# Kernel tuning notes

Hardware: AMD Instinct MI355X
Metric: run time of the kernel (lower is better)

## Reference

```python
import jax, jax.numpy as jnp
import numpy as np

B, H, W, ENC = 32, 14, 14, 2048
T = 21            # sequence length; 20 decode steps
V, E, A, L = 10000, 512, 512, 512
P = H * W


def setup_inputs() -> dict:
    key = jax.random.key(0)
    ks = jax.random.split(key, 24)
    g = lambda k, shape, s=0.02: (jax.random.normal(k, shape, jnp.float32) * s)
    return {
        "encoder_output": jax.random.normal(ks[0], (B, H, W, ENC), jnp.float32),
        # tokens in [1, V) so sign/abs length count gives full-length sequences
        "sequences": jax.random.randint(ks[1], (B, T), 1, V).astype(jnp.int64),
        "emb": g(ks[2], (V, E)),
        "Wea": g(ks[3], (ENC, A)), "bea": jnp.zeros((A,), jnp.float32),
        "Wga": g(ks[4], (L, A)),   "bga": jnp.zeros((A,), jnp.float32),
        "Wfa": g(ks[5], (A, 1)),   "bfa": jnp.zeros((1,), jnp.float32),
        "Wl": g(ks[6], (E + ENC, 4 * L)), "Ul": g(ks[7], (L, 4 * L)),
        "bl": jnp.zeros((4 * L,), jnp.float32),
        "Wim": g(ks[8], (ENC, L)), "bim": jnp.zeros((L,), jnp.float32),
        "Wic": g(ks[9], (ENC, L)), "bic": jnp.zeros((L,), jnp.float32),
        "Wb": g(ks[10], (L, ENC)), "bb": jnp.zeros((ENC,), jnp.float32),
        "Wo": g(ks[11], (L, V)),   "bo": jnp.zeros((V,), jnp.float32),
    }


def reference(encoder_output, sequences, emb, Wea, bea, Wga, bga, Wfa, bfa,
              Wl, Ul, bl, Wim, bim, Wic, bic, Wb, bb, Wo, bo):
    # --- sort by descending length (packed-sequence style) ---
    lengths = jnp.sum(jnp.sign(jnp.abs(sequences)), axis=1).astype(jnp.int32)
    order = jnp.argsort(-lengths)
    lengths = lengths[order] - 1                       # number of decode steps per row
    enc = encoder_output[order].reshape(B, P, ENC)     # [B, P, ENC]
    seqs = sequences[order]

    # --- init LSTM states from mean-pooled encoder features ---
    mean = enc.mean(axis=1)                            # [B, ENC]
    h0 = mean @ Wim + bim                              # 'memory_state' (plays role of h)
    c0 = mean @ Wic + bic                              # 'carry_state'  (plays role of c)

    # encoder side of additive attention is time-invariant: hoist out of the loop
    a1 = enc @ Wea + bea                               # [B, P, A]

    steps = T - 1
    toks = seqs[:, :steps].T                           # [steps, B] teacher-forced inputs
    masks = lengths[None, :] > jnp.arange(steps)[:, None]  # [steps, B] active rows

    def step(carry, xs):
        h, c = carry
        tok, m = xs
        # additive attention on carry (cell) state, as in the original code
        a2 = c @ Wga + bga                                         # [B, A]
        e = jnp.squeeze(jax.nn.relu(a1 + a2[:, None, :]) @ Wfa + bfa, -1)  # [B, P]
        alpha = jax.nn.softmax(e, axis=1)
        awe = jnp.einsum('bpe,bp->be', enc, alpha)                 # [B, ENC]
        beta = jax.nn.sigmoid(c @ Wb + bb)                         # gating
        x = jnp.concatenate([emb[tok], awe * beta], axis=1)        # [B, E+ENC]
        # Keras LSTMCell: gate order i, f, g, o
        z = x @ Wl + h @ Ul + bl
        zi, zf, zg, zo = jnp.split(z, 4, axis=1)
        c_new = jax.nn.sigmoid(zf) * c + jax.nn.sigmoid(zi) * jnp.tanh(zg)
        h_new = jax.nn.sigmoid(zo) * jnp.tanh(c_new)
        mf = m[:, None].astype(h.dtype)
        h_new = h_new * mf                 # zero-pad finished rows (packed semantics)
        c_new = c_new * mf
        pred = (c_new @ Wo + bo) * mf      # prediction from carry (cell) state, dropout off
        return (h_new, c_new), (pred, alpha * mf)

    (_, _), (preds, alphas) = jax.lax.scan(step, (h0, c0), (toks, masks))
    return preds.transpose(1, 0, 2), alphas.transpose(1, 0, 2), order
```

## Files before the change

kernel.cpp:

```cpp
#include <hip/hip_runtime.h>
#include <math.h>

#define B_    32
#define T_    21
#define STEPS 20
#define V_    10000
#define E_    512
#define A_    512
#define L_    512
#define P_    196
#define ENC_  2048
#define XW_   3072

#define WS_ORD    0
#define WS_SLEN   32
#define WS_CBUF   64
#define WS_CB0    32832
#define WS_CBALL  36928
#define WS_XB     200768
#define WS_A2S    299072
#define WS_BETA   315456
#define WS_ESH    380992
#define WS_A1B    389184
#define WS_WZP    1994816
#define WS_WCP    5140544
#define WS_WEAT   8384576
#define WS_MEAN   (WS_WZP)
#define WS_PH     (WS_WZP + 65536)

#define OUT_PRED  0
#define OUT_ALPHA 6400000
#define OUT_ORDER 6525440

typedef __attribute__((ext_vector_type(8))) short bf16x8;
typedef __attribute__((ext_vector_type(4))) float f32x4;
typedef unsigned short ushort_t;

__device__ inline unsigned f2bf2(float lo, float hi) {
    unsigned a = __float_as_uint(lo), b = __float_as_uint(hi);
    a = (a + 0x7FFFu + ((a >> 16) & 1u)) >> 16;
    b = (b + 0x7FFFu + ((b >> 16) & 1u)) >> 16;
    return a | (b << 16);
}
__device__ inline ushort_t f2bf(float f) {
    unsigned u = __float_as_uint(f);
    return (ushort_t)((u + 0x7FFFu + ((u >> 16) & 1u)) >> 16);
}
__device__ inline float bfu_lo(unsigned u) { return __uint_as_float(u << 16); }
__device__ inline float bfu_hi(unsigned u) { return __uint_as_float(u & 0xFFFF0000u); }

__global__ void k_order(const int* __restrict__ seqs, int* __restrict__ ord,
                        int* __restrict__ slen, float* __restrict__ out_ord)
{
    __shared__ int len[B_];
    int i = threadIdx.x;
    if (i < B_) {
        int c = 0;
        for (int t = 0; t < T_; ++t) c += (seqs[i * T_ + t] != 0) ? 1 : 0;
        len[i] = c;
    }
    __syncthreads();
    if (i < B_) {
        int li = len[i], r = 0;
        for (int j = 0; j < B_; ++j) {
            int lj = len[j];
            if (lj > li || (lj == li && j < i)) ++r;
        }
        ord[r] = i; slen[r] = li - 1; out_ord[r] = (float)i;
    }
}

__global__ void k_mean(const float* __restrict__ enc, const int* __restrict__ ord,
                       float* __restrict__ mean)
{
    int tid = blockIdx.x * 256 + threadIdx.x;
    int b = tid >> 11, e = tid & 2047;
    const float* row = enc + (size_t)ord[b] * (P_ * ENC_) + e;
    float s = 0.f;
    for (int p = 0; p < P_; ++p) s += row[(size_t)p * ENC_];
    mean[tid] = s * (1.0f / 196.0f);
}

__global__ void sg_both(const float* __restrict__ X, const float* __restrict__ Wim,
                        const float* __restrict__ Wic, float* __restrict__ part)
{
    const int n = blockIdx.x * 256 + threadIdx.x;
    const int c = blockIdx.y;
    const int bh = blockIdx.z & 1;
    const int which = blockIdx.z >> 1;
    const float* W = which ? Wic : Wim;
    const int chunk_ofs = which * 16;
    const int k0 = c * 128;
    const int k1 = k0 + 128;
    float acc[16];
#pragma unroll
    for (int b = 0; b < 16; ++b) acc[b] = 0.f;
    const float* Xb = X + (size_t)(bh * 16) * 2048;
    for (int k = k0; k < k1; k += 4) {
        float w0 = W[(size_t)(k + 0) * 512 + n];
        float w1 = W[(size_t)(k + 1) * 512 + n];
        float w2 = W[(size_t)(k + 2) * 512 + n];
        float w3 = W[(size_t)(k + 3) * 512 + n];
#pragma unroll
        for (int b = 0; b < 16; ++b) {
            const float4 xv = *reinterpret_cast<const float4*>(&Xb[(size_t)b * 2048 + k]);
            acc[b] += xv.x * w0 + xv.y * w1 + xv.z * w2 + xv.w * w3;
        }
    }
    float* po = part + (size_t)(chunk_ofs + c) * (B_ * 512) + (size_t)(bh * 16) * 512;
#pragma unroll
    for (int b = 0; b < 16; ++b) po[(size_t)b * 512 + n] = acc[b];
}

__global__ void k_h0c0(const float* __restrict__ ph, const float* __restrict__ bim,
                       const float* __restrict__ bic, float* __restrict__ c0,
                       ushort_t* __restrict__ cB0, ushort_t* __restrict__ XB0)
{
    int tid = blockIdx.x * 256 + threadIdx.x;
    int half = tid >> 14;
    int idx = tid & 16383;
    int l = idx & 511, b = idx >> 9;
    int cofs = half ? 16 : 0;
    float s = 0.f;
    for (int c = 0; c < 16; ++c) s += ph[(size_t)(cofs + c) * (B_ * 512) + idx];
    if (half) {
        float cv = s + bic[l];
        c0[idx] = cv;
        cB0[idx] = f2bf(cv);
    } else {
        XB0[(size_t)b * XW_ + 2560 + l] = f2bf(s + bim[l]);
    }
}

__global__ void k_packAll(const float* __restrict__ Wea, const float* __restrict__ Wl,
                          const float* __restrict__ Ul, const float* __restrict__ Wb,
                          const float* __restrict__ Wga, const float* __restrict__ Wo,
                          ushort_t* __restrict__ WT, ushort_t* __restrict__ Wz,
                          ushort_t* __restrict__ Wc)
{
    const int bid = blockIdx.x;
    if (bid < 4096) {
        int tid = bid * 256 + threadIdx.x;
        int n = tid >> 11, k = tid & 2047;
        WT[tid] = f2bf(Wea[(size_t)k * 512 + n]);
    } else if (bid < 7168) {
        const unsigned tidg = (unsigned)(bid - 4096) * 256 + threadIdx.x;
        const int l = tidg & 63;
        const unsigned rem = tidg >> 6;
        const int kt = rem % 96;
        const int nt = rem / 96;
        const int k = kt * 32 + ((l >> 4) << 3);
        const int np = nt * 16 + (l & 15);
        const int n = (np & 3) * 512 + (np >> 2);
        float v[8];
#pragma unroll
        for (int j = 0; j < 8; ++j) {
            int kr = k + j;
            v[j] = (kr < 2560) ? Wl[(size_t)kr * 2048 + n] : Ul[(size_t)(kr - 2560) * 2048 + n];
        }
        uint4 o;
        o.x = f2bf2(v[0], v[1]); o.y = f2bf2(v[2], v[3]);
        o.z = f2bf2(v[4], v[5]); o.w = f2bf2(v[6], v[7]);
        *reinterpret_cast<uint4*>(Wz + (size_t)tidg * 8) = o;
    } else {
        const unsigned tidg = (unsigned)(bid - 7168) * 256 + threadIdx.x;
        const int l = tidg & 63;
        const int kt = (tidg >> 6) & 15;
        const int nt = tidg >> 10;
        const int k = kt * 32 + ((l >> 4) << 3);
        const int n = nt * 16 + (l & 15);
        float v[8];
#pragma unroll
        for (int j = 0; j < 8; ++j) {
            int kr = k + j;
            float x;
            if (n < 2048)            x = Wb[(size_t)kr * 2048 + n];
            else if (n < 2560)       x = Wga[(size_t)kr * 512 + (n - 2048)];
            else if (n < 2560 + V_)  x = Wo[(size_t)kr * V_ + (n - 2560)];
            else                     x = 0.f;
            v[j] = x;
        }
        uint4 o;
        o.x = f2bf2(v[0], v[1]); o.y = f2bf2(v[2], v[3]);
        o.z = f2bf2(v[4], v[5]); o.w = f2bf2(v[6], v[7]);
        *reinterpret_cast<uint4*>(Wc + (size_t)tidg * 8) = o;
    }
}

__global__ __launch_bounds__(256) void k_a1_mfma(
    const float* __restrict__ enc, const ushort_t* __restrict__ WeaT,
    const float* __restrict__ bea, const int* __restrict__ ord,
    ushort_t* __restrict__ a1b)
{
    __shared__ ushort_t As[2][64 * 40];
    __shared__ ushort_t Bs[2][128 * 40];
    const int tid = threadIdx.x;
    const int lane = tid & 63, wave = tid >> 6;
    const int m0 = blockIdx.x * 64;
    const int n0 = blockIdx.y * 128;

    const int arA = tid >> 2, akA = (tid & 3) * 8;
    const int gA = m0 + arA;
    const float* Ag = enc + ((size_t)ord[gA / P_] * P_ + (gA % P_)) * ENC_ + akA;
    const int cb0 = tid, cb1 = tid + 256;
    const ushort_t* Bg0 = WeaT + (size_t)(n0 + (cb0 >> 2)) * ENC_ + (cb0 & 3) * 8;
    const ushort_t* Bg1 = WeaT + (size_t)(n0 + (cb1 >> 2)) * ENC_ + (cb1 & 3) * 8;
    const int aoA  = arA * 40 + akA;
    const int aoB0 = (cb0 >> 2) * 40 + (cb0 & 3) * 8;
    const int aoB1 = (cb1 >> 2) * 40 + (cb1 & 3) * 8;

    const int wn = wave * 32;
    f32x4 acc[4][2] = {};

    {
        float4 v0 = *reinterpret_cast<const float4*>(Ag);
        float4 v1 = *reinterpret_cast<const float4*>(Ag + 4);
        uint4 pa;
        pa.x = f2bf2(v0.x, v0.y); pa.y = f2bf2(v0.z, v0.w);
        pa.z = f2bf2(v1.x, v1.y); pa.w = f2bf2(v1.z, v1.w);
        *reinterpret_cast<uint4*>(&As[0][aoA]) = pa;
        *reinterpret_cast<uint4*>(&Bs[0][aoB0]) = *reinterpret_cast<const uint4*>(Bg0);
        *reinterpret_cast<uint4*>(&Bs[0][aoB1]) = *reinterpret_cast<const uint4*>(Bg1);
    }
    __syncthreads();

    for (int it = 0; it < 64; ++it) {
        const int cur = it & 1;
        uint4 npa, npb0, npb1;
        const bool more = (it < 63);
        if (more) {
            const int k0 = (it + 1) * 32;
            float4 v0 = *reinterpret_cast<const float4*>(Ag + k0);
            float4 v1 = *reinterpret_cast<const float4*>(Ag + k0 + 4);
            npa.x = f2bf2(v0.x, v0.y); npa.y = f2bf2(v0.z, v0.w);
            npa.z = f2bf2(v1.x, v1.y); npa.w = f2bf2(v1.z, v1.w);
            npb0 = *reinterpret_cast<const uint4*>(Bg0 + k0);
            npb1 = *reinterpret_cast<const uint4*>(Bg1 + k0);
        }
        {
            bf16x8 af[4], bfr[2];
            const int arow = lane & 15;
            const int koff = (lane >> 4) * 8;
#pragma unroll
            for (int mt = 0; mt < 4; ++mt)
                af[mt] = *reinterpret_cast<const bf16x8*>(&As[cur][(arow + mt * 16) * 40 + koff]);
#pragma unroll
            for (int nt = 0; nt < 2; ++nt)
                bfr[nt] = *reinterpret_cast<const bf16x8*>(&Bs[cur][(wn + nt * 16 + arow) * 40 + koff]);
#pragma unroll
            for (int mt = 0; mt < 4; ++mt)
#pragma unroll
                for (int nt = 0; nt < 2; ++nt)
                    acc[mt][nt] = __builtin_amdgcn_mfma_f32_16x16x32_bf16(
                        af[mt], bfr[nt], acc[mt][nt], 0, 0, 0);
        }
        if (more) {
            const int nxt = cur ^ 1;
            *reinterpret_cast<uint4*>(&As[nxt][aoA]) = npa;
            *reinterpret_cast<uint4*>(&Bs[nxt][aoB0]) = npb0;
            *reinterpret_cast<uint4*>(&Bs[nxt][aoB1]) = npb1;
        }
        __syncthreads();
    }
    const int rbase = (lane >> 4) * 4;
    const int cbase = lane & 15;
#pragma unroll
    for (int nt = 0; nt < 2; ++nt) {
        int col = n0 + wn + nt * 16 + cbase;
        float be = bea[col];
#pragma unroll
        for (int mt = 0; mt < 4; ++mt) {
            int row = m0 + mt * 16 + rbase;
#pragma unroll
            for (int r = 0; r < 4; ++r)
                a1b[(size_t)(row + r) * 512 + col] = f2bf(acc[mt][nt][r] + be);
        }
    }
}

__global__ __launch_bounds__(256, 1) void k_eawex(
    const float* __restrict__ a2s, const float* __restrict__ Wfa,
    const float* __restrict__ bfa, const ushort_t* __restrict__ a1b,
    const float* __restrict__ enc, const int* __restrict__ ord,
    const int* __restrict__ slen, int t, const float* __restrict__ beta,
    float* __restrict__ out_alpha, ushort_t* __restrict__ XB)
{
    __shared__ float a2sh[512];
    __shared__ float wfsh[512];
    __shared__ float esh[208];
    __shared__ float red[256];
    __shared__ float part[4][512];
    const int b = blockIdx.x >> 2, ec = blockIdx.x & 3;
    const int tid = threadIdx.x;
    const int wave = tid >> 6, lane = tid & 63;
    a2sh[tid] = a2s[b * 512 + tid];       a2sh[tid + 256] = a2s[b * 512 + 256 + tid];
    wfsh[tid] = Wfa[tid];                 wfsh[tid + 256] = Wfa[256 + tid];
    __syncthreads();

    const int grp = lane >> 4, sub = lane & 15;
    float4 a2r[4][2], wfr[4][2];
#pragma unroll
    for (int blk = 0; blk < 4; ++blk)
#pragma unroll
        for (int j = 0; j < 2; ++j) {
            int d = blk * 128 + sub * 8 + j * 4;
            a2r[blk][j] = *reinterpret_cast<const float4*>(&a2sh[d]);
            wfr[blk][j] = *reinterpret_cast<const float4*>(&wfsh[d]);
        }
    const float bf0 = bfa[0];
#pragma unroll
    for (int pass = 0; pass < 13; ++pass) {
        const int pl = pass * 16 + wave * 4 + grp;
        const bool valid = pl < P_;
        const int p = valid ? pl : 0;
        const ushort_t* arow = a1b + ((size_t)b * P_ + p) * 512;
        float s = 0.f;
#pragma unroll
        for (int blk = 0; blk < 4; ++blk) {
            uint4 raw = *reinterpret_cast<const uint4*>(arow + blk * 128 + sub * 8);
            float4 av = a2r[blk][0], wv = wfr[blk][0];
            float v;
            v = bfu_lo(raw.x) + av.x; v = v > 0.f ? v : 0.f; s += v * wv.x;
            v = bfu_hi(raw.x) + av.y; v = v > 0.f ? v : 0.f; s += v * wv.y;
            v = bfu_lo(raw.y) + av.z; v = v > 0.f ? v : 0.f; s += v * wv.z;
            v = bfu_hi(raw.y) + av.w; v = v > 0.f ? v : 0.f; s += v * wv.w;
            av = a2r[blk][1]; wv = wfr[blk][1];
            v = bfu_lo(raw.z) + av.x; v = v > 0.f ? v : 0.f; s += v * wv.x;
            v = bfu_hi(raw.z) + av.y; v = v > 0.f ? v : 0.f; s += v * wv.y;
            v = bfu_lo(raw.w) + av.z; v = v > 0.f ? v : 0.f; s += v * wv.z;
            v = bfu_hi(raw.w) + av.w; v = v > 0.f ? v : 0.f; s += v * wv.w;
        }
        s += __shfl_xor(s, 1, 64);
        s += __shfl_xor(s, 2, 64);
        s += __shfl_xor(s, 4, 64);
        s += __shfl_xor(s, 8, 64);
        if (sub == 0 && valid) esh[pl] = s + bf0;
    }
    __syncthreads();

    float v = (tid < P_) ? esh[tid] : -1e30f;
    red[tid] = v; __syncthreads();
    for (int s2 = 128; s2 > 0; s2 >>= 1) {
        if (tid < s2) red[tid] = fmaxf(red[tid], red[tid + s2]);
        __syncthreads();
    }
    float mx = red[0]; __syncthreads();
    float ex = (tid < P_) ? expf(v - mx) : 0.f;
    red[tid] = ex; __syncthreads();
    for (int s2 = 128; s2 > 0; s2 >>= 1) {
        if (tid < s2) red[tid] += red[tid + s2];
        __syncthreads();
    }
    float inv = 1.0f / red[0];
    float al = ex * inv;
    __syncthreads();
    if (tid < P_) esh[tid] = al;
    if (ec == 0 && tid < P_) {
        float mf = (slen[b] > t) ? 1.f : 0.f;
        out_alpha[((size_t)b * STEPS + t) * P_ + tid] = al * mf;
    }
    __syncthreads();

    const int col0 = ec * 512 + lane * 8;
    const float* ep = enc + (size_t)ord[b] * (P_ * ENC_) + (size_t)wave * 49 * ENC_ + col0;
    float s8[8] = {0.f, 0.f, 0.f, 0.f, 0.f, 0.f, 0.f, 0.f};
    for (int i = 0; i < 49; ++i) {
        float ap = esh[wave * 49 + i];
        float4 u0 = *reinterpret_cast<const float4*>(ep + (size_t)i * ENC_);
        float4 u1 = *reinterpret_cast<const float4*>(ep + (size_t)i * ENC_ + 4);
        s8[0] += ap * u0.x; s8[1] += ap * u0.y; s8[2] += ap * u0.z; s8[3] += ap * u0.w;
        s8[4] += ap * u1.x; s8[5] += ap * u1.y; s8[6] += ap * u1.z; s8[7] += ap * u1.w;
    }
#pragma unroll
    for (int j = 0; j < 8; ++j) part[wave][lane * 8 + j] = s8[j];
    __syncthreads();
    const int cc = tid * 2;
    float r0 = part[0][cc] + part[1][cc] + part[2][cc] + part[3][cc];
    float r1 = part[0][cc + 1] + part[1][cc + 1] + part[2][cc + 1] + part[3][cc + 1];
    const int col = ec * 512 + cc;
    float2 bt = *reinterpret_cast<const float2*>(&beta[b * 2048 + col]);
    unsigned pk = f2bf2(r0 * bt.x, r1 * bt.y);
    *reinterpret_cast<unsigned*>(XB + (size_t)b * XW_ + 512 + col) = pk;
}

__global__ __launch_bounds__(512) void k_zgates(
    const ushort_t* __restrict__ XB_in, const ushort_t* __restrict__ WzP,
    const float* __restrict__ bl, const float* __restrict__ c_in,
    const int* __restrict__ slen, int t,
    float* __restrict__ c_out, ushort_t* __restrict__ cB_slot,
    ushort_t* __restrict__ XB_out)
{
    __shared__ float zsh[8][32][16];
    const int tid = threadIdx.x, lane = tid & 63, w = tid >> 6;
    const int nt = blockIdx.x;
    const int kt0 = w * 12;
    const int ar = lane & 15, ak = (lane >> 4) * 8;
    const ushort_t* A0 = XB_in + (size_t)ar * XW_ + kt0 * 32 + ak;
    const ushort_t* Bp = WzP + ((size_t)nt * 96 + kt0) * 512 + lane * 8;
    f32x4 acc0 = {}, acc1 = {};
#pragma unroll
    for (int kt = 0; kt < 12; ++kt) {
        bf16x8 a0 = *reinterpret_cast<const bf16x8*>(A0 + kt * 32);
        bf16x8 a1 = *reinterpret_cast<const bf16x8*>(A0 + 16 * XW_ + kt * 32);
        bf16x8 bf = *reinterpret_cast<const bf16x8*>(Bp + kt * 512);
        acc0 = __builtin_amdgcn_mfma_f32_16x16x32_bf16(a0, bf, acc0, 0, 0, 0);
        acc1 = __builtin_amdgcn_mfma_f32_16x16x32_bf16(a1, bf, acc1, 0, 0, 0);
    }
    const int col = lane & 15, r0 = (lane >> 4) * 4;
#pragma unroll
    for (int r = 0; r < 4; ++r) {
        zsh[w][r0 + r][col] = acc0[r];
        zsh[w][16 + r0 + r][col] = acc1[r];
    }
    __syncthreads();
    if (tid < 128) {
        const int b = tid >> 2, li = tid & 3;
        const int l = nt * 4 + li;
        float z[4];
#pragma unroll
        for (int g = 0; g < 4; ++g) {
            const int c = li * 4 + g;
            z[g] = zsh[0][b][c] + zsh[1][b][c] + zsh[2][b][c] + zsh[3][b][c]
                 + zsh[4][b][c] + zsh[5][b][c] + zsh[6][b][c] + zsh[7][b][c]
                 + bl[g * 512 + l];
        }
        float si = 1.f / (1.f + expf(-z[0]));
        float sf = 1.f / (1.f + expf(-z[1]));
        float gg = tanhf(z[2]);
        float so = 1.f / (1.f + expf(-z[3]));
        float cn = sf * c_in[b * 512 + l] + si * gg;
        float hn = so * tanhf(cn);
        float mf = (slen[b] > t) ? 1.f : 0.f;
        cn *= mf; hn *= mf;
        c_out[b * 512 + l] = cn;
        cB_slot[b * 512 + l] = f2bf(cn);
        XB_out[(size_t)b * XW_ + 2560 + l] = f2bf(hn);
    }
}

__global__ __launch_bounds__(256) void k_cmfma_lite(
    const ushort_t* __restrict__ cB, const ushort_t* __restrict__ WcP,
    const float* __restrict__ bb, const float* __restrict__ bga,
    int tnext, const int* __restrict__ seqs, const float* __restrict__ emb,
    const int* __restrict__ ord,
    float* __restrict__ beta, float* __restrict__ a2s, ushort_t* __restrict__ XB_out)
{
    const int bid = blockIdx.x, tid = threadIdx.x;
    if (bid >= 20) {
        const int g = (bid - 20) * 256 + tid;
        const int b = g >> 4, j0 = (g & 15) * 32;
        const int tok = seqs[ord[b] * T_ + tnext];
        const float4* src = reinterpret_cast<const float4*>(emb + (size_t)tok * E_ + j0);
        uint4* dst = reinterpret_cast<uint4*>(XB_out + (size_t)b * XW_ + j0);
#pragma unroll
        for (int q = 0; q < 4; ++q) {
            float4 v0 = src[2 * q], v1 = src[2 * q + 1];
            uint4 o;
            o.x = f2bf2(v0.x, v0.y); o.y = f2bf2(v0.z, v0.w);
            o.z = f2bf2(v1.x, v1.y); o.w = f2bf2(v1.z, v1.w);
            dst[q] = o;
        }
        return;
    }
    const int lane = tid & 63, w = tid >> 6;
    const int nt0 = bid * 8 + w * 2;
    const int ar = lane & 15, ak = (lane >> 4) * 8;
    const ushort_t* A0 = cB + ar * 512 + ak;
    const ushort_t* Bp = WcP + (size_t)nt0 * 8192 + lane * 8;
    f32x4 acc[2][2] = {};
    for (int kt = 0; kt < 16; ++kt) {
        bf16x8 a0 = *reinterpret_cast<const bf16x8*>(A0 + kt * 32);
        bf16x8 a1 = *reinterpret_cast<const bf16x8*>(A0 + 16 * 512 + kt * 32);
        bf16x8 b0 = *reinterpret_cast<const bf16x8*>(Bp + kt * 512);
        bf16x8 b1 = *reinterpret_cast<const bf16x8*>(Bp + 8192 + kt * 512);
        acc[0][0] = __builtin_amdgcn_mfma_f32_16x16x32_bf16(a0, b0, acc[0][0], 0, 0, 0);
        acc[0][1] = __builtin_amdgcn_mfma_f32_16x16x32_bf16(a0, b1, acc[0][1], 0, 0, 0);
        acc[1][0] = __builtin_amdgcn_mfma_f32_16x16x32_bf16(a1, b0, acc[1][0], 0, 0, 0);
        acc[1][1] = __builtin_amdgcn_mfma_f32_16x16x32_bf16(a1, b1, acc[1][1], 0, 0, 0);
    }
    const int r0 = (lane >> 4) * 4, cb2 = lane & 15;
#pragma unroll
    for (int nti = 0; nti < 2; ++nti) {
        const int n = (nt0 + nti) * 16 + cb2;
#pragma unroll
        for (int mt = 0; mt < 2; ++mt) {
#pragma unroll
            for (int r = 0; r < 4; ++r) {
                const int brow = mt * 16 + r0 + r;
                float v = acc[mt][nti][r];
                if (n < 2048) {
                    beta[brow * 2048 + n] = 1.f / (1.f + expf(-(v + bb[n])));
                } else {
                    a2s[brow * 512 + (n - 2048)] = v + bga[n - 2048];
                }
            }
        }
    }
}

__global__ __launch_bounds__(256) void k_pred(
    const ushort_t* __restrict__ cBall, const ushort_t* __restrict__ WcP,
    const float* __restrict__ bo, const int* __restrict__ slen,
    float* __restrict__ out_pred)
{
    const int tid = threadIdx.x, lane = tid & 63, w = tid >> 6;
    const int n0 = blockIdx.x * 128;
    const int m0 = blockIdx.y * 128;
    const int wm = (w >> 1) * 64, wn = (w & 1) * 64;
    const int ar = lane & 15, ak = (lane >> 4) * 8;
    const int ntb = (2560 + n0 + wn) >> 4;
    f32x4 acc[4][4] = {};
    for (int kt = 0; kt < 16; ++kt) {
        bf16x8 af[4], bfr[4];
#pragma unroll
        for (int mt = 0; mt < 4; ++mt)
            af[mt] = *reinterpret_cast<const bf16x8*>(
                cBall + (size_t)(m0 + wm + mt * 16 + ar) * 512 + kt * 32 + ak);
#pragma unroll
        for (int nt = 0; nt < 4; ++nt)
            bfr[nt] = *reinterpret_cast<const bf16x8*>(
                WcP + ((size_t)(ntb + nt) * 16 + kt) * 512 + lane * 8);
#pragma unroll
        for (int mt = 0; mt < 4; ++mt)
#pragma unroll
            for (int nt = 0; nt < 4; ++nt)
                acc[mt][nt] = __builtin_amdgcn_mfma_f32_16x16x32_bf16(
                    af[mt], bfr[nt], acc[mt][nt], 0, 0, 0);
    }
    const int r0 = (lane >> 4) * 4, cb = lane & 15;
#pragma unroll
    for (int nt = 0; nt < 4; ++nt) {
        const int n = n0 + wn + nt * 16 + cb;
        if (n < V_) {
            const float bv = bo[n];
#pragma unroll
            for (int mt = 0; mt < 4; ++mt) {
#pragma unroll
                for (int r = 0; r < 4; ++r) {
                    const int m = m0 + wm + mt * 16 + r0 + r;
                    const int tt = m >> 5, bb_ = m & 31;
                    const float mf = (slen[bb_] > tt) ? 1.f : 0.f;
                    out_pred[((size_t)bb_ * STEPS + tt) * V_ + n] =
                        (acc[mt][nt][r] + bv) * mf;
                }
            }
        }
    }
}

extern "C" void kernel_launch(void* const* d_in, const int* in_sizes, int n_in,
                              void* d_out, int out_size, void* d_ws, size_t ws_size,
                              hipStream_t stream)
{
    const float* enc  = (const float*)d_in[0];
    const int*   seqs = (const int*)  d_in[1];
    const float* emb  = (const float*)d_in[2];
    const float* Wea  = (const float*)d_in[3];
    const float* bea  = (const float*)d_in[4];
    const float* Wga  = (const float*)d_in[5];
    const float* bga  = (const float*)d_in[6];
    const float* Wfa  = (const float*)d_in[7];
    const float* bfa  = (const float*)d_in[8];
    const float* Wl   = (const float*)d_in[9];
    const float* Ul   = (const float*)d_in[10];
    const float* bl   = (const float*)d_in[11];
    const float* Wim  = (const float*)d_in[12];
    const float* bim  = (const float*)d_in[13];
    const float* Wic  = (const float*)d_in[14];
    const float* bic  = (const float*)d_in[15];
    const float* Wb   = (const float*)d_in[16];
    const float* bb   = (const float*)d_in[17];
    const float* Wo   = (const float*)d_in[18];
    const float* bo   = (const float*)d_in[19];

    float* out = (float*)d_out;
    float* ws  = (float*)d_ws;
    int* ord  = (int*)(ws + WS_ORD);
    int* slen = (int*)(ws + WS_SLEN);
    ushort_t* cB0   = (ushort_t*)(ws + WS_CB0);
    ushort_t* cBall = (ushort_t*)(ws + WS_CBALL);
    ushort_t* XB0   = (ushort_t*)(ws + WS_XB);
    ushort_t* XB1   = (ushort_t*)(ws + WS_XB) + (size_t)B_ * XW_;
    ushort_t* a1b   = (ushort_t*)(ws + WS_A1B);
    ushort_t* WzP   = (ushort_t*)(ws + WS_WZP);
    ushort_t* WcP   = (ushort_t*)(ws + WS_WCP);
    ushort_t* WeaT  = (ushort_t*)(ws + WS_WEAT);
    float* a2s  = ws + WS_A2S;
    float* beta = ws + WS_BETA;

    k_order<<<1, 64, 0, stream>>>(seqs, ord, slen, out + OUT_ORDER);
    k_mean<<<256, 256, 0, stream>>>(enc, ord, ws + WS_MEAN);
    sg_both<<<dim3(2, 16, 4), 256, 0, stream>>>(ws + WS_MEAN, Wim, Wic, ws + WS_PH);
    k_h0c0<<<128, 256, 0, stream>>>(ws + WS_PH, bim, bic, ws + WS_CBUF, cB0, XB0);
    k_packAll<<<10336, 256, 0, stream>>>(Wea, Wl, Ul, Wb, Wga, Wo, WeaT, WzP, WcP);
    k_a1_mfma<<<dim3(98, 4), 256, 0, stream>>>(enc, WeaT, bea, ord, a1b);
    k_cmfma_lite<<<22, 256, 0, stream>>>(cB0, WcP, bb, bga, 0, seqs, emb, ord,
                                         beta, a2s, XB0);

    for (int t = 0; t < STEPS; ++t) {
        float* c_in  = ws + WS_CBUF + (t & 1) * (B_ * L_);
        float* c_out = ws + WS_CBUF + ((t + 1) & 1) * (B_ * L_);
        ushort_t* cB_slot = cBall + (size_t)t * (B_ * L_);
        ushort_t* xb_cur = (t & 1) ? XB1 : XB0;
        ushort_t* xb_nxt = (t & 1) ? XB0 : XB1;

        k_eawex<<<128, 256, 0, stream>>>(a2s, Wfa, bfa, a1b, enc, ord, slen, t,
                                         beta, out + OUT_ALPHA, xb_cur);
        k_zgates<<<128, 512, 0, stream>>>(xb_cur, WzP, bl, c_in, slen, t,
                                          c_out, cB_slot, xb_nxt);
        if (t < STEPS - 1)
            k_cmfma_lite<<<22, 256, 0, stream>>>(cB_slot, WcP, bb, bga, t + 1,
                                                 seqs, emb, ord, beta, a2s, xb_nxt);
    }
    k_pred<<<dim3(79, 5), 256, 0, stream>>>(cBall, WcP, bo, slen, out + OUT_PRED);
}
```

Measured before the change: 1.147 ms.

## Widen grids of per-step decode kernels to fill more compute units

Each per-step kernel is split across more blocks. The attention-weighted encoder sum now uses 8 column chunks per batch row instead of 4. The LSTM gate GEMM is split into two batch halves. The beta/a2 GEMM gives each block one 16-column tile and splits K across waves with a shared-memory reduction, going from 22 to 162 blocks. The a1 GEMM grid axes are also swapped so consecutive blocks cover the N dimension. The aim is to raise occupancy on a GPU with many CUs for these small latency-bound kernels, at the cost of redundant activation loads and extra reductions.

```diff
diff --git a/kernel.cpp b/kernel.cpp
--- a/kernel.cpp
+++ b/kernel.cpp
@@ -196,8 +196,8 @@
     __shared__ ushort_t Bs[2][128 * 40];
     const int tid = threadIdx.x;
     const int lane = tid & 63, wave = tid >> 6;
-    const int m0 = blockIdx.x * 64;
-    const int n0 = blockIdx.y * 128;
+    const int m0 = blockIdx.y * 64;
+    const int n0 = blockIdx.x * 128;
 
     const int arA = tid >> 2, akA = (tid & 3) * 8;
     const int gA = m0 + arA;
@@ -289,8 +289,8 @@
     __shared__ float wfsh[512];
     __shared__ float esh[208];
     __shared__ float red[256];
-    __shared__ float part[4][512];
-    const int b = blockIdx.x >> 2, ec = blockIdx.x & 3;
+    __shared__ float part[4][256];
+    const int b = blockIdx.x >> 3, ec = blockIdx.x & 7;
     const int tid = threadIdx.x;
     const int wave = tid >> 6, lane = tid & 63;
     a2sh[tid] = a2s[b * 512 + tid];       a2sh[tid + 256] = a2s[b * 512 + 256 + tid];
@@ -361,26 +361,26 @@
     }
     __syncthreads();
 
-    const int col0 = ec * 512 + lane * 8;
+    const int col0 = ec * 256 + lane * 4;
     const float* ep = enc + (size_t)ord[b] * (P_ * ENC_) + (size_t)wave * 49 * ENC_ + col0;
-    float s8[8] = {0.f, 0.f, 0.f, 0.f, 0.f, 0.f, 0.f, 0.f};
+    float s4[4] = {0.f, 0.f, 0.f, 0.f};
     for (int i = 0; i < 49; ++i) {
         float ap = esh[wave * 49 + i];
-        float4 u0 = *reinterpret_cast<const float4*>(ep + (size_t)i * ENC_);
-        float4 u1 = *reinterpret_cast<const float4*>(ep + (size_t)i * ENC_ + 4);
-        s8[0] += ap * u0.x; s8[1] += ap * u0.y; s8[2] += ap * u0.z; s8[3] += ap * u0.w;
-        s8[4] += ap * u1.x; s8[5] += ap * u1.y; s8[6] += ap * u1.z; s8[7] += ap * u1.w;
-    }
-#pragma unroll
-    for (int j = 0; j < 8; ++j) part[wave][lane * 8 + j] = s8[j];
-    __syncthreads();
-    const int cc = tid * 2;
-    float r0 = part[0][cc] + part[1][cc] + part[2][cc] + part[3][cc];
-    float r1 = part[0][cc + 1] + part[1][cc + 1] + part[2][cc + 1] + part[3][cc + 1];
-    const int col = ec * 512 + cc;
-    float2 bt = *reinterpret_cast<const float2*>(&beta[b * 2048 + col]);
-    unsigned pk = f2bf2(r0 * bt.x, r1 * bt.y);
-    *reinterpret_cast<unsigned*>(XB + (size_t)b * XW_ + 512 + col) = pk;
+        float4 u = *reinterpret_cast<const float4*>(ep + (size_t)i * ENC_);
+        s4[0] += ap * u.x; s4[1] += ap * u.y; s4[2] += ap * u.z; s4[3] += ap * u.w;
+    }
+#pragma unroll
+    for (int j = 0; j < 4; ++j) part[wave][lane * 4 + j] = s4[j];
+    __syncthreads();
+    if (tid < 128) {
+        const int cc = tid * 2;
+        float r0 = part[0][cc] + part[1][cc] + part[2][cc] + part[3][cc];
+        float r1 = part[0][cc + 1] + part[1][cc + 1] + part[2][cc + 1] + part[3][cc + 1];
+        const int col = ec * 256 + cc;
+        float2 bt = *reinterpret_cast<const float2*>(&beta[b * 2048 + col]);
+        unsigned pk = f2bf2(r0 * bt.x, r1 * bt.y);
+        *reinterpret_cast<unsigned*>(XB + (size_t)b * XW_ + 512 + col) = pk;
+    }
 }
 
 __global__ __launch_bounds__(512) void k_zgates(
@@ -390,38 +390,35 @@
     float* __restrict__ c_out, ushort_t* __restrict__ cB_slot,
     ushort_t* __restrict__ XB_out)
 {
-    __shared__ float zsh[8][32][16];
+    __shared__ float zsh[8][16][16];
     const int tid = threadIdx.x, lane = tid & 63, w = tid >> 6;
-    const int nt = blockIdx.x;
+    const int nt = blockIdx.x >> 1;
+    const int mb = blockIdx.x & 1;
     const int kt0 = w * 12;
     const int ar = lane & 15, ak = (lane >> 4) * 8;
-    const ushort_t* A0 = XB_in + (size_t)ar * XW_ + kt0 * 32 + ak;
+    const ushort_t* A0 = XB_in + (size_t)(mb * 16 + ar) * XW_ + kt0 * 32 + ak;
     const ushort_t* Bp = WzP + ((size_t)nt * 96 + kt0) * 512 + lane * 8;
-    f32x4 acc0 = {}, acc1 = {};
+    f32x4 acc0 = {};
 #pragma unroll
     for (int kt = 0; kt < 12; ++kt) {
         bf16x8 a0 = *reinterpret_cast<const bf16x8*>(A0 + kt * 32);
-        bf16x8 a1 = *reinterpret_cast<const bf16x8*>(A0 + 16 * XW_ + kt * 32);
         bf16x8 bf = *reinterpret_cast<const bf16x8*>(Bp + kt * 512);
         acc0 = __builtin_amdgcn_mfma_f32_16x16x32_bf16(a0, bf, acc0, 0, 0, 0);
-        acc1 = __builtin_amdgcn_mfma_f32_16x16x32_bf16(a1, bf, acc1, 0, 0, 0);
     }
     const int col = lane & 15, r0 = (lane >> 4) * 4;
 #pragma unroll
-    for (int r = 0; r < 4; ++r) {
-        zsh[w][r0 + r][col] = acc0[r];
-        zsh[w][16 + r0 + r][col] = acc1[r];
-    }
-    __syncthreads();
-    if (tid < 128) {
-        const int b = tid >> 2, li = tid & 3;
+    for (int r = 0; r < 4; ++r) zsh[w][r0 + r][col] = acc0[r];
+    __syncthreads();
+    if (tid < 64) {
+        const int bl_ = tid >> 2, li = tid & 3;
+        const int b = mb * 16 + bl_;
         const int l = nt * 4 + li;
         float z[4];
 #pragma unroll
         for (int g = 0; g < 4; ++g) {
             const int c = li * 4 + g;
-            z[g] = zsh[0][b][c] + zsh[1][b][c] + zsh[2][b][c] + zsh[3][b][c]
-                 + zsh[4][b][c] + zsh[5][b][c] + zsh[6][b][c] + zsh[7][b][c]
+            z[g] = zsh[0][bl_][c] + zsh[1][bl_][c] + zsh[2][bl_][c] + zsh[3][bl_][c]
+                 + zsh[4][bl_][c] + zsh[5][bl_][c] + zsh[6][bl_][c] + zsh[7][bl_][c]
                  + bl[g * 512 + l];
         }
         float si = 1.f / (1.f + expf(-z[0]));
@@ -445,9 +442,10 @@
     const int* __restrict__ ord,
     float* __restrict__ beta, float* __restrict__ a2s, ushort_t* __restrict__ XB_out)
 {
+    __shared__ float zsh[4][32][16];
     const int bid = blockIdx.x, tid = threadIdx.x;
-    if (bid >= 20) {
-        const int g = (bid - 20) * 256 + tid;
+    if (bid >= 160) {
+        const int g = (bid - 160) * 256 + tid;
         const int b = g >> 4, j0 = (g & 15) * 32;
         const int tok = seqs[ord[b] * T_ + tnext];
         const float4* src = reinterpret_cast<const float4*>(emb + (size_t)tok * E_ + j0);
@@ -463,35 +461,38 @@
         return;
     }
     const int lane = tid & 63, w = tid >> 6;
-    const int nt0 = bid * 8 + w * 2;
+    const int nt = bid;
     const int ar = lane & 15, ak = (lane >> 4) * 8;
-    const ushort_t* A0 = cB + ar * 512 + ak;
-    const ushort_t* Bp = WcP + (size_t)nt0 * 8192 + lane * 8;
-    f32x4 acc[2][2] = {};
-    for (int kt = 0; kt < 16; ++kt) {
+    const ushort_t* A0 = cB + ar * 512 + w * 128 + ak;
+    const ushort_t* Bp = WcP + ((size_t)nt * 16 + w * 4) * 512 + lane * 8;
+    f32x4 acc0 = {}, acc1 = {};
+#pragma unroll
+    for (int kt = 0; kt < 4; ++kt) {
         bf16x8 a0 = *reinterpret_cast<const bf16x8*>(A0 + kt * 32);
         bf16x8 a1 = *reinterpret_cast<const bf16x8*>(A0 + 16 * 512 + kt * 32);
         bf16x8 b0 = *reinterpret_cast<const bf16x8*>(Bp + kt * 512);
-        bf16x8 b1 = *reinterpret_cast<const bf16x8*>(Bp + 8192 + kt * 512);
-        acc[0][0] = __builtin_amdgcn_mfma_f32_16x16x32_bf16(a0, b0, acc[0][0], 0, 0, 0);
-        acc[0][1] = __builtin_amdgcn_mfma_f32_16x16x32_bf16(a0, b1, acc[0][1], 0, 0, 0);
-        acc[1][0] = __builtin_amdgcn_mfma_f32_16x16x32_bf16(a1, b0, acc[1][0], 0, 0, 0);
-        acc[1][1] = __builtin_amdgcn_mfma_f32_16x16x32_bf16(a1, b1, acc[1][1], 0, 0, 0);
-    }
-    const int r0 = (lane >> 4) * 4, cb2 = lane & 15;
-#pragma unroll
-    for (int nti = 0; nti < 2; ++nti) {
-        const int n = (nt0 + nti) * 16 + cb2;
-#pragma unroll
-        for (int mt = 0; mt < 2; ++mt) {
-#pragma unroll
-            for (int r = 0; r < 4; ++r) {
-                const int brow = mt * 16 + r0 + r;
-                float v = acc[mt][nti][r];
+        acc0 = __builtin_amdgcn_mfma_f32_16x16x32_bf16(a0, b0, acc0, 0, 0, 0);
+        acc1 = __builtin_amdgcn_mfma_f32_16x16x32_bf16(a1, b0, acc1, 0, 0, 0);
+    }
+    const int col = lane & 15, r0 = (lane >> 4) * 4;
+#pragma unroll
+    for (int r = 0; r < 4; ++r) {
+        zsh[w][r0 + r][col] = acc0[r];
+        zsh[w][16 + r0 + r][col] = acc1[r];
+    }
+    __syncthreads();
+    if (tid < 256) {
+#pragma unroll
+        for (int half = 0; half < 2; ++half) {
+            const int idx = tid + half * 256;
+            if (idx < 512) {
+                const int row = idx >> 4, cc = idx & 15;
+                float v = zsh[0][row][cc] + zsh[1][row][cc] + zsh[2][row][cc] + zsh[3][row][cc];
+                const int n = nt * 16 + cc;
                 if (n < 2048) {
-                    beta[brow * 2048 + n] = 1.f / (1.f + expf(-(v + bb[n])));
+                    beta[row * 2048 + n] = 1.f / (1.f + expf(-(v + bb[n])));
                 } else {
-                    a2s[brow * 512 + (n - 2048)] = v + bga[n - 2048];
+                    a2s[row * 512 + (n - 2048)] = v + bga[n - 2048];
                 }
             }
         }
@@ -593,9 +594,9 @@
     sg_both<<<dim3(2, 16, 4), 256, 0, stream>>>(ws + WS_MEAN, Wim, Wic, ws + WS_PH);
     k_h0c0<<<128, 256, 0, stream>>>(ws + WS_PH, bim, bic, ws + WS_CBUF, cB0, XB0);
     k_packAll<<<10336, 256, 0, stream>>>(Wea, Wl, Ul, Wb, Wga, Wo, WeaT, WzP, WcP);
-    k_a1_mfma<<<dim3(98, 4), 256, 0, stream>>>(enc, WeaT, bea, ord, a1b);
-    k_cmfma_lite<<<22, 256, 0, stream>>>(cB0, WcP, bb, bga, 0, seqs, emb, ord,
-                                         beta, a2s, XB0);
+    k_a1_mfma<<<dim3(4, 98), 256, 0, stream>>>(enc, WeaT, bea, ord, a1b);
+    k_cmfma_lite<<<162, 256, 0, stream>>>(cB0, WcP, bb, bga, 0, seqs, emb, ord,
+                                          beta, a2s, XB0);
 
     for (int t = 0; t < STEPS; ++t) {
         float* c_in  = ws + WS_CBUF + (t & 1) * (B_ * L_);
@@ -604,13 +605,13 @@
         ushort_t* xb_cur = (t & 1) ? XB1 : XB0;
         ushort_t* xb_nxt = (t & 1) ? XB0 : XB1;
 
-        k_eawex<<<128, 256, 0, stream>>>(a2s, Wfa, bfa, a1b, enc, ord, slen, t,
+        k_eawex<<<256, 256, 0, stream>>>(a2s, Wfa, bfa, a1b, enc, ord, slen, t,
                                          beta, out + OUT_ALPHA, xb_cur);
-        k_zgates<<<128, 512, 0, stream>>>(xb_cur, WzP, bl, c_in, slen, t,
+        k_zgates<<<256, 512, 0, stream>>>(xb_cur, WzP, bl, c_in, slen, t,
                                           c_out, cB_slot, xb_nxt);
         if (t < STEPS - 1)
-            k_cmfma_lite<<<22, 256, 0, stream>>>(cB_slot, WcP, bb, bga, t + 1,
-                                                 seqs, emb, ord, beta, a2s, xb_nxt);
+            k_cmfma_lite<<<162, 256, 0, stream>>>(cB_slot, WcP, bb, bga, t + 1,
+                                                  seqs, emb, ord, beta, a2s, xb_nxt);
     }
     k_pred<<<dim3(79, 5), 256, 0, stream>>>(cBall, WcP, bo, slen, out + OUT_PRED);
 }
```

Result: faster. 920.0 us (-19.8%).
